# Kernel tuning notes

Measured on AMD Instinct MI355X. Metric: run time of the kernel, lower is better.

Reference implementation:

```python
import jax, jax.numpy as jnp
import numpy as np

# Config (lite version of KimiK2): 2 layers, dim 2048, 16 heads x 128, MLA latent rank 512,
# 4 experts / top-2, SwiGLU inter dim 1024, vocab 32000, batch 2, seq 1024.
DEPTH, DIM, H, HD, R, DFF, E, TOPK, V, B, S = 2, 2048, 16, 128, 512, 1024, 4, 2, 32000, 2, 1024
EPS = 1e-6


def rmsnorm(x, w):
    var = jnp.mean(jnp.square(x), axis=-1, keepdims=True)
    return x * jax.lax.rsqrt(var + EPS) * w


def setup_inputs() -> dict:
    key = jax.random.key(0)
    ks = jax.random.split(key, 16)
    sd = 0.02
    d = {
        'x_tokens': jax.random.randint(ks[0], (B, S), 0, V),
        'emb': jax.random.normal(ks[1], (V, DIM), jnp.float32) * sd,
        'embed_norm_w': jnp.ones((DIM,), jnp.float32),
        # per-layer stacked params (leading axis DEPTH)
        'norm_w': jnp.ones((DEPTH, DIM), jnp.float32),
        'Wq': jax.random.normal(ks[2], (DEPTH, DIM, H * HD), jnp.float32) * sd,
        'Wdkv': jax.random.normal(ks[3], (DEPTH, DIM, R), jnp.float32) * sd,
        'Wuk': jax.random.normal(ks[4], (DEPTH, R, H * HD), jnp.float32) * sd,
        'Wuv': jax.random.normal(ks[5], (DEPTH, R, H * HD), jnp.float32) * sd,
        'Wo': jax.random.normal(ks[6], (DEPTH, H * HD, DIM), jnp.float32) * sd,
        'Wg': jax.random.normal(ks[7], (DEPTH, DIM, E), jnp.float32) * sd,
        'W1': jax.random.normal(ks[8], (DEPTH, E, DIM, DFF), jnp.float32) * sd,
        'W3': jax.random.normal(ks[9], (DEPTH, E, DIM, DFF), jnp.float32) * sd,
        'W2': jax.random.normal(ks[10], (DEPTH, E, DFF, DIM), jnp.float32) * sd,
        'head_norm_w': jnp.ones((DIM,), jnp.float32),
        'head_W': jax.random.normal(ks[11], (DIM, V), jnp.float32) * sd,
        'head_b': jnp.zeros((V,), jnp.float32),
    }
    return d


def mla(x, Wq, Wdkv, Wuk, Wuv, Wo):
    # Multi-head latent attention: queries from x, K/V from a low-rank latent c.
    Bq, Sq, _ = x.shape
    q = (x @ Wq).reshape(Bq, Sq, H, HD)
    c = x @ Wdkv                                   # [B,S,R] compressed KV latent
    k = (c @ Wuk).reshape(Bq, Sq, H, HD)
    v = (c @ Wuv).reshape(Bq, Sq, H, HD)
    scores = jnp.einsum('bqhd,bkhd->bhqk', q, k) / jnp.sqrt(jnp.float32(HD))
    a = jax.nn.softmax(scores, axis=-1)            # block never passes a mask -> full attention
    o = jnp.einsum('bhqk,bkhd->bqhd', a, v).reshape(Bq, Sq, H * HD)
    return o @ Wo


def moe(x, Wg, W1, W3, W2):
    # x: [B,S,D] -> flatten tokens. Dense-over-experts (E=4) with top-k masked gates.
    Bq, Sq, Dq = x.shape
    xt = x.reshape(Bq * Sq, Dq)                    # [T,D]
    gate = jax.nn.softmax(xt @ Wg, axis=-1)        # [T,E]
    topv, topi = jax.lax.top_k(gate, TOPK)
    topv = topv / jnp.sum(topv, axis=-1, keepdims=True)
    gw = jnp.zeros_like(gate).at[jnp.arange(xt.shape[0])[:, None], topi].set(topv)  # [T,E]
    h = jnp.einsum('td,edf->etf', xt, W1)
    g = jnp.einsum('td,edf->etf', xt, W3)
    eo = jnp.einsum('etf,efd->etd', jax.nn.silu(h) * g, W2)
    out = jnp.einsum('etd,te->td', eo, gw)
    return out.reshape(Bq, Sq, Dq)


def reference(x_tokens, emb, embed_norm_w, norm_w, Wq, Wdkv, Wuk, Wuv, Wo, Wg, W1, W3, W2, head_norm_w, head_W, head_b):
    h = emb[x_tokens]
    h = rmsnorm(h, embed_norm_w)

    def layer(h, p):
        nw, wq, wdkv, wuk, wuv, wo, wg, w1, w3, w2 = p
        h = h + mla(rmsnorm(h, nw), wq, wdkv, wuk, wuv, wo)
        # NOTE: same norm weight reused pre-MoE, as in the torch module
        h = h + moe(rmsnorm(h, nw), wg, w1, w3, w2)
        return h, None

    h, _ = jax.lax.scan(layer, h, (norm_w, Wq, Wdkv, Wuk, Wuv, Wo, Wg, W1, W3, W2))
    return rmsnorm(h, head_norm_w) @ head_W + head_b
```

## Files before the change

kernel.cpp:

```cpp
#include <hip/hip_runtime.h>
#include <hip/hip_bf16.h>

typedef __hip_bfloat16 bf16;
typedef __bf16 bf16x8 __attribute__((ext_vector_type(8)));
typedef float f32x4 __attribute__((ext_vector_type(4)));
typedef unsigned short u16;
typedef unsigned int u32;
typedef __attribute__((address_space(1))) const void* gptr_t;
typedef __attribute__((address_space(3))) void* lptr_t;

static constexpr int TOKS = 2048, DM = 2048, RL = 512, DF = 1024, SQ = 1024, NV = 32000;
static constexpr int CAP = 1536;
static constexpr long PL_X  = (long)TOKS * DM;
static constexpr long PL_C  = (long)TOKS * RL;
static constexpr long PL_VT = 2l * 16 * 128 * 1024;
static constexpr long M4 = 4l * 1024 * 1024;
static constexpr long M2 = 2l * 1024 * 1024;

__device__ __forceinline__ float b2f(bf16 x){ return __bfloat162float(x); }
__device__ __forceinline__ bf16  f2b(float x){ return __float2bfloat16(x); }
__device__ __forceinline__ void split1(float x, u16& h, u16& l){
  bf16 hb = f2b(x);
  float r = x - b2f(hb);
  bf16 lb = f2b(r);
  h = *(u16*)&hb; l = *(u16*)&lb;
}

__device__ __forceinline__ float block_red(float v, int op){
  __shared__ float red[4];
  const int lane = threadIdx.x & 63, wv = threadIdx.x >> 6;
  #pragma unroll
  for (int off = 32; off > 0; off >>= 1){
    float o = __shfl_down(v, off, 64);
    v = op ? fmaxf(v, o) : v + o;
  }
  __syncthreads();
  if (lane == 0) red[wv] = v;
  __syncthreads();
  float r = red[0];
  #pragma unroll
  for (int i = 1; i < 4; ++i) r = op ? fmaxf(r, red[i]) : r + red[i];
  return r;
}

__global__ __launch_bounds__(256)
void embed_norm_k(const int* __restrict__ toks, const float* __restrict__ emb,
                  const float* __restrict__ w, float* __restrict__ h){
  const int t = blockIdx.x;
  const long tok = toks[t];
  const int base = threadIdx.x * 8;
  const float* ep = emb + tok * (long)DM + base;
  float4 va = *(const float4*)ep, vb = *(const float4*)(ep + 4);
  float v[8] = {va.x, va.y, va.z, va.w, vb.x, vb.y, vb.z, vb.w};
  float ss = 0.f;
  #pragma unroll
  for (int i = 0; i < 8; ++i) ss += v[i]*v[i];
  ss = block_red(ss, 0);
  const float inv = rsqrtf(ss / DM + 1e-6f);
  float4 wa = *(const float4*)(w + base), wb4 = *(const float4*)(w + base + 4);
  float wv[8] = {wa.x, wa.y, wa.z, wa.w, wb4.x, wb4.y, wb4.z, wb4.w};
  float* hp = h + (long)t * DM + base;
  #pragma unroll
  for (int i = 0; i < 8; ++i) hp[i] = v[i] * inv * wv[i];
}

__global__ __launch_bounds__(256)
void rmsnorm_planes_k(const float* __restrict__ h, const float* __restrict__ w,
                      u16* __restrict__ hi, u16* __restrict__ lo){
  const int t = blockIdx.x;
  const int base = threadIdx.x * 8;
  const float* hp = h + (long)t * DM + base;
  float4 va = *(const float4*)hp, vb = *(const float4*)(hp + 4);
  float v[8] = {va.x, va.y, va.z, va.w, vb.x, vb.y, vb.z, vb.w};
  float ss = 0.f;
  #pragma unroll
  for (int i = 0; i < 8; ++i) ss += v[i]*v[i];
  ss = block_red(ss, 0);
  const float inv = rsqrtf(ss / DM + 1e-6f);
  float4 wa = *(const float4*)(w + base), wb4 = *(const float4*)(w + base + 4);
  float wv[8] = {wa.x, wa.y, wa.z, wa.w, wb4.x, wb4.y, wb4.z, wb4.w};
  u16 hvv[8], lvv[8];
  #pragma unroll
  for (int i = 0; i < 8; ++i) split1(v[i] * inv * wv[i], hvv[i], lvv[i]);
  *(int4*)(hi + (long)t * DM + base) = *(const int4*)hvv;
  *(int4*)(lo + (long)t * DM + base) = *(const int4*)lvv;
}

__global__ __launch_bounds__(256)
void gate_k(const float* __restrict__ h, const float* __restrict__ nw,
            const float* __restrict__ Wg, float* __restrict__ gw){
  const int t = blockIdx.x;
  const int base = threadIdx.x * 8;
  const float* hp = h + (long)t * DM + base;
  float4 va = *(const float4*)hp, vb = *(const float4*)(hp + 4);
  float v[8] = {va.x, va.y, va.z, va.w, vb.x, vb.y, vb.z, vb.w};
  float ss = 0.f;
  #pragma unroll
  for (int i = 0; i < 8; ++i) ss += v[i]*v[i];
  ss = block_red(ss, 0);
  const float inv = rsqrtf(ss / DM + 1e-6f);
  float a[4] = {0.f, 0.f, 0.f, 0.f};
  #pragma unroll
  for (int i = 0; i < 8; ++i){
    const float xv = v[i] * inv * nw[base + i];
    #pragma unroll
    for (int e = 0; e < 4; ++e) a[e] += xv * Wg[(base + i)*4 + e];
  }
  #pragma unroll
  for (int e = 0; e < 4; ++e) a[e] = block_red(a[e], 0);
  if (threadIdx.x == 0){
    int i1 = 0;
    for (int e = 1; e < 4; ++e) if (a[e] > a[i1]) i1 = e;
    int i2 = -1;
    for (int e = 0; e < 4; ++e){ if (e == i1) continue; if (i2 < 0 || a[e] > a[i2]) i2 = e; }
    float g[4];
    const float m = fmaxf(fmaxf(a[0], a[1]), fmaxf(a[2], a[3]));
    float s = 0.f;
    for (int e = 0; e < 4; ++e){ g[e] = __expf(a[e] - m); s += g[e]; }
    for (int e = 0; e < 4; ++e) g[e] /= s;
    const float ns = g[i1] + g[i2];
    float* op = gw + (long)t * 4;
    op[0] = 0.f; op[1] = 0.f; op[2] = 0.f; op[3] = 0.f;
    op[i1] = g[i1] / ns; op[i2] = g[i2] / ns;
  }
}

__global__ __launch_bounds__(256)
void build_lists_k(const float* __restrict__ gw, int* __restrict__ idx, int* __restrict__ cnt){
  const int e = threadIdx.x >> 6, lane = threadIdx.x & 63;
  int base = 0;
  for (int t0 = 0; t0 < TOKS; t0 += 64){
    const int t = t0 + lane;
    const bool sel = gw[(long)t * 4 + e] > 0.f;
    const unsigned long long m = __ballot(sel);
    const int pos = __popcll(m & ((1ull << lane) - 1ull));
    if (sel && base + pos < CAP) idx[e * CAP + base + pos] = t;
    base += (int)__popcll(m);
  }
  if (lane == 0) cnt[e] = base < CAP ? base : CAP;
}

__global__ __launch_bounds__(256)
void gather2_k(const u16* __restrict__ xph, const int* __restrict__ idx,
               const int* __restrict__ cnt, int ebase, u16* __restrict__ xg){
  const int e = blockIdx.x / CAP, r = blockIdx.x % CAP;
  if (r >= cnt[ebase + e]) return;
  const long t = idx[(long)(ebase + e) * CAP + r];
  const int c = threadIdx.x * 8;
  const long dst = ((long)e * 2 * CAP + r) * DM + c;
  *(int4*)(xg + dst) = *(const int4*)(xph + t * DM + c);
  *(int4*)(xg + dst + (long)CAP * DM) = *(const int4*)(xph + PL_X + t * DM + c);
}

__global__ __launch_bounds__(256)
void gatherb_k(const u16* __restrict__ xph, const int* __restrict__ idx,
               const int* __restrict__ cnt, u16* __restrict__ xgb){
  const int e = blockIdx.x / CAP, r = blockIdx.x % CAP;
  if (r >= cnt[e]) return;
  const long t = idx[(long)e * CAP + r];
  const int c = threadIdx.x * 8;
  *(int4*)(xgb + ((long)e * CAP + r) * DM + c) = *(const int4*)(xph + t * DM + c);
}

__global__ __launch_bounds__(256)
void softmax_pack_k(float* __restrict__ pf){
  const long row = blockIdx.x;
  const float* pr = pf + row * SQ;
  const int base = threadIdx.x * 4;
  float4 v4 = *(const float4*)(pr + base);
  float v[4] = {v4.x, v4.y, v4.z, v4.w};
  float m = fmaxf(fmaxf(v[0], v[1]), fmaxf(v[2], v[3]));
  m = block_red(m, 1);
  float s = 0.f;
  #pragma unroll
  for (int i = 0; i < 4; ++i){ v[i] = __expf(v[i] - m); s += v[i]; }
  s = block_red(s, 0);
  const float inv = 1.f / s;
  u16 hv[4], lv[4];
  #pragma unroll
  for (int i = 0; i < 4; ++i) split1(v[i] * inv, hv[i], lv[i]);
  u16* out = (u16*)pf + row * 2048;
  *(int2*)(out + base) = *(const int2*)hv;
  *(int2*)(out + 1024 + base) = *(const int2*)lv;
}

__global__ __launch_bounds__(256)
void swiglu_pack_k(float* __restrict__ h1, const float* __restrict__ h3){
  const int t = threadIdx.x;
  const long r = (long)blockIdx.x * 2 + (t >> 7);
  const int col = (t & 127) * 8;
  const float* p1 = h1 + r * 1024 + col;
  const float* p3 = h3 + r * 1024 + col;
  float4 a0 = *(const float4*)p1, a1 = *(const float4*)(p1 + 4);
  float4 b0 = *(const float4*)p3, b1 = *(const float4*)(p3 + 4);
  float a[8] = {a0.x, a0.y, a0.z, a0.w, a1.x, a1.y, a1.z, a1.w};
  float b[8] = {b0.x, b0.y, b0.z, b0.w, b1.x, b1.y, b1.z, b1.w};
  u16 hv[8], lv[8];
  #pragma unroll
  for (int j = 0; j < 8; ++j){
    const float y = (a[j] / (1.f + __expf(-a[j]))) * b[j];
    split1(y, hv[j], lv[j]);
  }
  __syncthreads();
  u16* out = (u16*)h1 + r * 2048;
  *(int4*)(out + col) = *(const int4*)hv;
  *(int4*)(out + 1024 + col) = *(const int4*)lv;
}

__global__ __launch_bounds__(256)
void swiglu_bk(bf16* __restrict__ h1, const bf16* __restrict__ h3){
  const long i = ((long)blockIdx.x * 256 + threadIdx.x) * 8;
  union { int4 i4; bf16 b[8]; } x, y;
  x.i4 = *(const int4*)(h1 + i);
  y.i4 = *(const int4*)(h3 + i);
  #pragma unroll
  for (int j = 0; j < 8; ++j){
    const float a = b2f(x.b[j]);
    const float b = b2f(y.b[j]);
    x.b[j] = f2b((a / (1.f + __expf(-a))) * b);
  }
  *(int4*)(h1 + i) = x.i4;
}

__global__ __launch_bounds__(256)
void tsplit_k(const float* __restrict__ in, long inz, int ldin,
              u16* __restrict__ oh, u16* __restrict__ ol, long outz, int ldout, int ntx){
  __shared__ u16 lh[64][72], ll[64][72];
  const int z = blockIdx.z;
  in += (long)z * inz; oh += (long)z * outz; ol += (long)z * outz;
  const int bx = blockIdx.x % ntx, by = blockIdx.x / ntx;
  const int k0 = by * 64, n0 = bx * 64;
  const int t = threadIdx.x;
  {
    const int r = t >> 2, cb = (t & 3) * 16;
    const float* ip = in + (long)(k0 + r) * ldin + n0 + cb;
    #pragma unroll
    for (int i = 0; i < 16; i += 4){
      float4 v = *(const float4*)(ip + i);
      float a[4] = {v.x, v.y, v.z, v.w};
      #pragma unroll
      for (int j = 0; j < 4; ++j){
        u16 hv, lv; split1(a[j], hv, lv);
        lh[r][cb + i + j] = hv; ll[r][cb + i + j] = lv;
      }
    }
  }
  __syncthreads();
  {
    const int n = t >> 2, kb = (t & 3) * 16;
    u16 hv[16], lv[16];
    #pragma unroll
    for (int i = 0; i < 16; ++i){ hv[i] = lh[kb + i][n]; lv[i] = ll[kb + i][n]; }
    u16* po = oh + (long)(n0 + n) * ldout + k0 + kb;
    u16* pl = ol + (long)(n0 + n) * ldout + k0 + kb;
    *(int4*)po = *(const int4*)hv; *(int4*)(po + 8) = *(const int4*)(hv + 8);
    *(int4*)pl = *(const int4*)lv; *(int4*)(pl + 8) = *(const int4*)(lv + 8);
  }
}

__global__ __launch_bounds__(256)
void tconv_k(const float* __restrict__ in, long inz, int ldin,
             bf16* __restrict__ out, long outz, int ldout, int ntx){
  __shared__ u16 lh[64][72];
  const int z = blockIdx.z;
  in += (long)z * inz; out += (long)z * outz;
  const int bx = blockIdx.x % ntx, by = blockIdx.x / ntx;
  const int k0 = by * 64, n0 = bx * 64;
  const int t = threadIdx.x;
  {
    const int r = t >> 2, cb = (t & 3) * 16;
    const float* ip = in + (long)(k0 + r) * ldin + n0 + cb;
    #pragma unroll
    for (int i = 0; i < 16; i += 4){
      float4 v = *(const float4*)(ip + i);
      float a[4] = {v.x, v.y, v.z, v.w};
      #pragma unroll
      for (int j = 0; j < 4; ++j){ bf16 hb = f2b(a[j]); lh[r][cb + i + j] = *(u16*)&hb; }
    }
  }
  __syncthreads();
  {
    const int n = t >> 2, kb = (t & 3) * 16;
    u16 hv[16];
    #pragma unroll
    for (int i = 0; i < 16; ++i) hv[i] = lh[kb + i][n];
    u16* po = (u16*)out + (long)(n0 + n) * ldout + k0 + kb;
    *(int4*)po = *(const int4*)hv; *(int4*)(po + 8) = *(const int4*)(hv + 8);
  }
}

__device__ __forceinline__ int swz64(int r, int c){
  return ((((c >> 3) + r) & 7) << 3) | (c & 7);
}
__device__ __forceinline__ int swz2(int r, int c){
  return ((((c >> 3) + (r >> 1)) & 3) << 3) | (c & 7);
}
__device__ __forceinline__ int2 tile_xy(int ny){
  const int nwg = gridDim.x;
  const int wid = blockIdx.x;
  const int q = nwg >> 3, r = nwg & 7;
  const int xcd = wid & 7, pos = wid >> 3;
  const int lid = (xcd < r) ? (xcd*(q+1) + pos) : (r*(q+1) + (xcd - r)*q + pos);
  return make_int2(lid / ny, lid % ny);
}

__device__ __forceinline__ void stage64(const u16* src, int ld, int rbase, int k0,
                                        u16* lp, int sub, int lane){
  const int r = sub * 8 + (lane >> 3);
  const int cs = ((lane & 7) - r) & 7;
  const u16* g = src + (long)(rbase + r) * ld + k0 + cs * 8;
  __builtin_amdgcn_global_load_lds((gptr_t)g, (lptr_t)(lp + sub * 512), 16, 0, 0);
}
__device__ __forceinline__ void stage32(const u16* src, int ld, int rbase, int k0,
                                        u16* lp, int sub, int lane){
  const int r = sub * 16 + (lane >> 2);
  const int cs = ((lane & 3) - (r >> 1)) & 3;
  const u16* g = src + (long)(rbase + r) * ld + k0 + cs * 8;
  __builtin_amdgcn_global_load_lds((gptr_t)g, (lptr_t)(lp + sub * 512), 16, 0, 0);
}

template<int MT, int OM>
__global__ __launch_bounds__(256)
void gemms_nt(const u16* __restrict__ Ah, const u16* __restrict__ Al, long ab, int lda,
              const u16* __restrict__ Bh, const u16* __restrict__ Bl, long bb, int ldb,
              void* __restrict__ Cv, long cb, int ldc, long cpl,
              int K, float scale, const float* __restrict__ aux, int gst, int ny,
              const int* __restrict__ rowmap, const int* __restrict__ cntp)
{
  __shared__ __align__(16) u16 ash[MT*32][64], asl[MT*32][64];
  __shared__ __align__(16) u16 bsh[128][64], bsl[128][64];
  const int z = blockIdx.z;
  Ah += (long)z * ab; Al += (long)z * ab;
  Bh += (long)z * bb; Bl += (long)z * bb;
  const int2 tt = tile_xy(ny);
  const int m0 = tt.y * (MT*32), n0 = tt.x * 128;
  int cntv = 1 << 30;
  if (cntp){ cntv = cntp[z]; if (m0 >= cntv) return; }
  const int tid = threadIdx.x, lane = tid & 63, wv = tid >> 6;
  const int wr = (wv >> 1) * (MT*16), wc = (wv & 1) * 64;
  const int fr = lane & 15, fk = (lane >> 4) * 8;

  f32x4 acc[MT][4] = {};
  constexpr int AI4 = MT * 4;

  for (int k0 = 0; k0 < K; k0 += 64){
    __syncthreads();
    #pragma unroll
    for (int ii = 0; ii < 2*AI4 + 32; ++ii){
      if ((ii & 3) != wv) continue;
      if (ii < AI4)             stage64(Ah, lda, m0, k0, &ash[0][0], ii, lane);
      else if (ii < 2*AI4)      stage64(Al, lda, m0, k0, &asl[0][0], ii - AI4, lane);
      else if (ii < 2*AI4 + 16) stage64(Bh, ldb, n0, k0, &bsh[0][0], ii - 2*AI4, lane);
      else                      stage64(Bl, ldb, n0, k0, &bsl[0][0], ii - 2*AI4 - 16, lane);
    }
    __syncthreads();
    bf16x8 ahf[MT][2], alf[MT][2], bhf[4][2], blf[4][2];
    #pragma unroll
    for (int mi = 0; mi < MT; ++mi){
      const int rr = wr + mi * 16 + fr;
      #pragma unroll
      for (int ks = 0; ks < 2; ++ks){
        const int sc = swz64(rr, ks * 32 + fk);
        ahf[mi][ks] = *(const bf16x8*)&ash[rr][sc];
        alf[mi][ks] = *(const bf16x8*)&asl[rr][sc];
      }
    }
    #pragma unroll
    for (int ni = 0; ni < 4; ++ni){
      const int rr = wc + ni * 16 + fr;
      #pragma unroll
      for (int ks = 0; ks < 2; ++ks){
        const int sc = swz64(rr, ks * 32 + fk);
        bhf[ni][ks] = *(const bf16x8*)&bsh[rr][sc];
        blf[ni][ks] = *(const bf16x8*)&bsl[rr][sc];
      }
    }
    #pragma unroll
    for (int mi = 0; mi < MT; ++mi)
      #pragma unroll
      for (int ni = 0; ni < 4; ++ni)
        #pragma unroll
        for (int ks = 0; ks < 2; ++ks){
          acc[mi][ni] = __builtin_amdgcn_mfma_f32_16x16x32_bf16(ahf[mi][ks], bhf[ni][ks], acc[mi][ni], 0, 0, 0);
          acc[mi][ni] = __builtin_amdgcn_mfma_f32_16x16x32_bf16(ahf[mi][ks], blf[ni][ks], acc[mi][ni], 0, 0, 0);
          acc[mi][ni] = __builtin_amdgcn_mfma_f32_16x16x32_bf16(alf[mi][ks], bhf[ni][ks], acc[mi][ni], 0, 0, 0);
        }
  }

  const int crow = (lane >> 4) * 4, ccol = lane & 15;
  #pragma unroll
  for (int mi = 0; mi < MT; ++mi){
    #pragma unroll
    for (int ni = 0; ni < 4; ++ni){
      const int gm0 = m0 + wr + mi * 16 + crow;
      const int gn = n0 + wc + ni * 16 + ccol;
      if (OM == 5){
        u16 hv[4], lv[4];
        #pragma unroll
        for (int j = 0; j < 4; ++j) split1(acc[mi][ni][j], hv[j], lv[j]);
        const long off = (((long)(gm0 >> 10) * 16 + (gn >> 7)) * 128 + (gn & 127)) * 1024 + (gm0 & 1023);
        u16* vt = (u16*)Cv;
        *(int2*)(vt + off) = *(const int2*)hv;
        *(int2*)(vt + cpl + off) = *(const int2*)lv;
      } else if (OM == 6){
        #pragma unroll
        for (int j = 0; j < 4; ++j){
          const int row = gm0 + j;
          if (row < cntv){
            const long t = rowmap[(long)z * CAP + row];
            ((float*)Cv)[t * ldc + gn] += aux[t * gst] * acc[mi][ni][j];
          }
        }
      } else {
        #pragma unroll
        for (int j = 0; j < 4; ++j){
          const long off = (long)z * cb + (long)(gm0 + j) * ldc + gn;
          const float v = acc[mi][ni][j];
          if (OM == 0)      ((float*)Cv)[off] = v * scale;
          else if (OM == 1) ((float*)Cv)[off] += v;
          else if (OM == 3) ((float*)Cv)[off] += aux[(long)(gm0 + j) * gst] * v;
          else { u16 hv, lv; split1(v, hv, lv); ((u16*)Cv)[off] = hv; ((u16*)Cv)[off + cpl] = lv; }
        }
      }
    }
  }
}

template<int MT, int OM>
__global__ __launch_bounds__(256)
void gemmb_nt(const bf16* __restrict__ A, long ab, int lda,
              const bf16* __restrict__ B, long bb, int ldb,
              void* __restrict__ Cv, long cb, int ldc,
              int K, const float* __restrict__ aux, int gst, int ny,
              const int* __restrict__ rowmap, const int* __restrict__ cntp)
{
  __shared__ __align__(16) u16 a_lds[MT*32][32];
  __shared__ __align__(16) u16 b_lds[128][32];
  const int z = blockIdx.z;
  A += (long)z * ab; B += (long)z * bb;
  const int2 tt = tile_xy(ny);
  const int m0 = tt.y * (MT*32), n0 = tt.x * 128;
  int cntv = 1 << 30;
  if (cntp){ cntv = cntp[z]; if (m0 >= cntv) return; }
  const int tid = threadIdx.x, lane = tid & 63, wv = tid >> 6;
  const int wr = (wv >> 1) * (MT*16), wc = (wv & 1) * 64;
  const int fr = lane & 15, fk = (lane >> 4) * 8;

  f32x4 acc[MT][4] = {};
  constexpr int AI = MT * 2;

  for (int k0 = 0; k0 < K; k0 += 32){
    __syncthreads();
    #pragma unroll
    for (int ii = 0; ii < AI + 8; ++ii){
      if ((ii & 3) != wv) continue;
      if (ii < AI) stage32((const u16*)A, lda, m0, k0, &a_lds[0][0], ii, lane);
      else         stage32((const u16*)B, ldb, n0, k0, &b_lds[0][0], ii - AI, lane);
    }
    __syncthreads();
    bf16x8 af[MT], bfv[4];
    #pragma unroll
    for (int mi = 0; mi < MT; ++mi){
      const int rr = wr + mi * 16 + fr;
      af[mi] = *(const bf16x8*)&a_lds[rr][swz2(rr, fk)];
    }
    #pragma unroll
    for (int ni = 0; ni < 4; ++ni){
      const int rr = wc + ni * 16 + fr;
      bfv[ni] = *(const bf16x8*)&b_lds[rr][swz2(rr, fk)];
    }
    #pragma unroll
    for (int mi = 0; mi < MT; ++mi)
      #pragma unroll
      for (int ni = 0; ni < 4; ++ni)
        acc[mi][ni] = __builtin_amdgcn_mfma_f32_16x16x32_bf16(af[mi], bfv[ni], acc[mi][ni], 0, 0, 0);
  }

  const int crow = (lane >> 4) * 4, ccol = lane & 15;
  #pragma unroll
  for (int mi = 0; mi < MT; ++mi){
    #pragma unroll
    for (int ni = 0; ni < 4; ++ni){
      const int gm0 = m0 + wr + mi * 16 + crow;
      const int gn = n0 + wc + ni * 16 + ccol;
      #pragma unroll
      for (int j = 0; j < 4; ++j){
        const float v = acc[mi][ni][j];
        if (OM == 7){
          const int row = gm0 + j;
          if (row < cntv){
            const long t = rowmap[(long)z * CAP + row];
            atomicAdd(&((float*)Cv)[t * ldc + gn], aux[t * gst + z] * v);
          }
        } else {
          const long off = (long)z * cb + (long)(gm0 + j) * ldc + gn;
          if (OM == 0)      ((bf16*)Cv)[off] = f2b(v);
          else if (OM == 2) ((float*)Cv)[off] = v + aux[gn];
          else              atomicAdd(&((float*)Cv)[off], aux[(long)(gm0 + j) * gst + z] * v);
        }
      }
    }
  }
}

extern "C" void kernel_launch(void* const* d_in, const int* in_sizes, int n_in,
                              void* d_out, int out_size, void* d_ws, size_t ws_size,
                              hipStream_t stream)
{
  (void)in_sizes; (void)n_in; (void)out_size; (void)ws_size;
  const int*   toks = (const int*)d_in[0];
  const float* emb  = (const float*)d_in[1];
  const float* enw  = (const float*)d_in[2];
  const float* nw   = (const float*)d_in[3];
  const float* Wq   = (const float*)d_in[4];
  const float* Wdkv = (const float*)d_in[5];
  const float* Wuk  = (const float*)d_in[6];
  const float* Wuv  = (const float*)d_in[7];
  const float* Wo   = (const float*)d_in[8];
  const float* Wg   = (const float*)d_in[9];
  const float* W1   = (const float*)d_in[10];
  const float* W3   = (const float*)d_in[11];
  const float* W2   = (const float*)d_in[12];
  const float* hnw  = (const float*)d_in[13];
  const float* hW   = (const float*)d_in[14];
  const float* hb   = (const float*)d_in[15];

  const size_t MB = 1ull << 20;
  char* ws = (char*)d_ws;
  float* h    = (float*)(ws);
  float* gw   = (float*)(ws + 16*MB);
  int*   idx  = (int*)(ws + 16*MB + 128*1024);
  int*   cnt  = (int*)(ws + 16*MB + 256*1024);
  u16*   xph  = (u16*)(ws + 17*MB);
  u16*   wpl  = (u16*)(ws + 33*MB);
  u16*   qph  = (u16*)(ws + 49*MB);
  u16*   cph  = (u16*)(ws + 65*MB);
  u16*   kph  = (u16*)(ws + 69*MB);
  u16*   vtp  = (u16*)(ws + 85*MB);
  u16*   oph  = (u16*)(ws + 101*MB);
  float* pf   = (float*)(ws + 17*MB);
  u16*   xg   = (u16*)(ws + 49*MB);
  float* h1f  = (float*)(ws + 73*MB);
  float* h3f  = (float*)(ws + 85*MB);
  bf16*  wT   = (bf16*)(ws + 33*MB);
  u16*   xgb  = (u16*)(ws + 49*MB);
  bf16*  h1b  = (bf16*)(ws + 73*MB);
  bf16*  h3b  = (bf16*)(ws + 85*MB);
  bf16*  whT  = (bf16*)(ws + 33*MB);

  const float qscale = 0.08838834764831845f;

  embed_norm_k<<<TOKS, 256, 0, stream>>>(toks, emb, enw, h);

  for (int l = 0; l < 2; ++l){
    const float* nwl = nw + (long)l * DM;
    rmsnorm_planes_k<<<TOKS, 256, 0, stream>>>(h, nwl, xph, xph + PL_X);

    tsplit_k<<<1024, 256, 0, stream>>>(Wq + (long)l*DM*DM, 0, DM, wpl, wpl + M4, 0, DM, 32);
    gemms_nt<2,4><<<dim3(512,1,1), 256, 0, stream>>>(xph, xph + PL_X, 0, DM, wpl, wpl + M4, 0, DM,
        qph, 0, DM, PL_X, DM, 1.f, nullptr, 0, 32, nullptr, nullptr);
    tsplit_k<<<256, 256, 0, stream>>>(Wdkv + (long)l*DM*RL, 0, RL, wpl, wpl + M2, 0, DM, 8);
    gemms_nt<2,4><<<dim3(128,1,1), 256, 0, stream>>>(xph, xph + PL_X, 0, DM, wpl, wpl + M2, 0, DM,
        cph, 0, RL, PL_C, DM, 1.f, nullptr, 0, 32, nullptr, nullptr);
    tsplit_k<<<256, 256, 0, stream>>>(Wuk + (long)l*RL*DM, 0, DM, wpl, wpl + M2, 0, RL, 32);
    gemms_nt<2,4><<<dim3(512,1,1), 256, 0, stream>>>(cph, cph + PL_C, 0, RL, wpl, wpl + M2, 0, RL,
        kph, 0, DM, PL_X, RL, 1.f, nullptr, 0, 32, nullptr, nullptr);
    tsplit_k<<<256, 256, 0, stream>>>(Wuv + (long)l*RL*DM, 0, DM, wpl, wpl + M2, 0, RL, 32);
    gemms_nt<2,5><<<dim3(512,1,1), 256, 0, stream>>>(cph, cph + PL_C, 0, RL, wpl, wpl + M2, 0, RL,
        vtp, 0, 0, PL_VT, RL, 1.f, nullptr, 0, 32, nullptr, nullptr);

    for (int b = 0; b < 2; ++b){
      for (int hg = 0; hg < 2; ++hg){
        const long qo = (long)b*SQ*DM + hg*1024;
        gemms_nt<4,0><<<dim3(64,1,8), 256, 0, stream>>>(qph + qo, qph + PL_X + qo, 128, DM,
            kph + qo, kph + PL_X + qo, 128, DM,
            pf, (long)SQ*SQ, SQ, 0, 128, qscale, nullptr, 0, 8, nullptr, nullptr);
        softmax_pack_k<<<8*SQ, 256, 0, stream>>>(pf);
        const long vo = ((long)b*16 + hg*8) * 128 * 1024;
        gemms_nt<1,4><<<dim3(32,1,8), 256, 0, stream>>>((const u16*)pf, (const u16*)pf + 1024,
            1024l*2048, 2048,
            vtp + vo, vtp + PL_VT + vo, 128l*1024, 1024,
            oph + (long)b*SQ*DM + hg*1024, 128, DM, PL_X, SQ, 1.f, nullptr, 0, 32, nullptr, nullptr);
      }
    }

    tsplit_k<<<1024, 256, 0, stream>>>(Wo + (long)l*DM*DM, 0, DM, wpl, wpl + M4, 0, DM, 32);
    gemms_nt<2,1><<<dim3(512,1,1), 256, 0, stream>>>(oph, oph + PL_X, 0, DM, wpl, wpl + M4, 0, DM,
        h, 0, DM, 0, DM, 1.f, nullptr, 0, 32, nullptr, nullptr);

    gate_k<<<TOKS, 256, 0, stream>>>(h, nwl, Wg + (long)l*DM*4, gw);
    build_lists_k<<<1, 256, 0, stream>>>(gw, idx, cnt);
    rmsnorm_planes_k<<<TOKS, 256, 0, stream>>>(h, nwl, xph, xph + PL_X);

    if (l == 0){
      for (int p2 = 0; p2 < 2; ++p2){
        const int ebase = p2 * 2;
        const long wo13 = ((long)l*4 + ebase) * (long)DM * DF;
        gather2_k<<<2*CAP, 256, 0, stream>>>(xph, idx, cnt, ebase, xg);
        tsplit_k<<<dim3(512,1,2), 256, 0, stream>>>(W1 + wo13, (long)DM*DF, DF, wpl, wpl + M4, M2, DM, 16);
        gemms_nt<2,0><<<dim3(192,1,2), 256, 0, stream>>>(xg, xg + (long)CAP*DM, 2l*CAP*DM, DM,
            wpl, wpl + M4, M2, DM, h1f, (long)CAP*DF, DF, 0, DM, 1.f, nullptr, 0, 24,
            nullptr, cnt + ebase);
        tsplit_k<<<dim3(512,1,2), 256, 0, stream>>>(W3 + wo13, (long)DM*DF, DF, wpl, wpl + M4, M2, DM, 16);
        gemms_nt<2,0><<<dim3(192,1,2), 256, 0, stream>>>(xg, xg + (long)CAP*DM, 2l*CAP*DM, DM,
            wpl, wpl + M4, M2, DM, h3f, (long)CAP*DF, DF, 0, DM, 1.f, nullptr, 0, 24,
            nullptr, cnt + ebase);
        swiglu_pack_k<<<CAP, 256, 0, stream>>>(h1f, h3f);
        tsplit_k<<<dim3(512,1,2), 256, 0, stream>>>(W2 + ((long)l*4 + ebase)*(long)DF*DM, (long)DF*DM, DM,
            wpl, wpl + M4, M2, DF, 32);
        for (int ei = 0; ei < 2; ++ei){
          gemms_nt<2,6><<<dim3(384,1,1), 256, 0, stream>>>(
              (const u16*)h1f + (long)ei*CAP*2048, (const u16*)h1f + (long)ei*CAP*2048 + 1024,
              0, 2048, wpl + (long)ei*M2, wpl + M4 + (long)ei*M2, 0, DF,
              h, 0, DM, 0, DF, 1.f, gw + ebase + ei, 4, 24,
              idx + (ebase + ei)*CAP, cnt + ebase + ei);
        }
      }
    } else {
      gatherb_k<<<4*CAP, 256, 0, stream>>>(xph, idx, cnt, xgb);
      tconv_k<<<dim3(512,1,4), 256, 0, stream>>>(W1 + (long)l*4*DM*DF, (long)DM*DF, DF, wT, M2, DM, 16);
      gemmb_nt<2,0><<<dim3(192,1,4), 256, 0, stream>>>((const bf16*)xgb, (long)CAP*DM, DM, wT, M2, DM,
          h1b, (long)CAP*DF, DF, DM, nullptr, 0, 24, nullptr, cnt);
      tconv_k<<<dim3(512,1,4), 256, 0, stream>>>(W3 + (long)l*4*DM*DF, (long)DM*DF, DF, wT, M2, DM, 16);
      gemmb_nt<2,0><<<dim3(192,1,4), 256, 0, stream>>>((const bf16*)xgb, (long)CAP*DM, DM, wT, M2, DM,
          h3b, (long)CAP*DF, DF, DM, nullptr, 0, 24, nullptr, cnt);
      swiglu_bk<<<(4*CAP*DF)/2048, 256, 0, stream>>>(h1b, h3b);
      tconv_k<<<dim3(512,1,4), 256, 0, stream>>>(W2 + (long)l*4*DF*DM, (long)DF*DM, DM, wT, M2, DF, 32);
      gemmb_nt<2,7><<<dim3(384,1,4), 256, 0, stream>>>(h1b, (long)CAP*DF, DF, wT, M2, DF,
          h, 0, DM, DF, gw, 4, 24, idx, cnt);
    }
  }

  rmsnorm_planes_k<<<TOKS, 256, 0, stream>>>(h, hnw, xph, xph + PL_X);
  for (int half = 0; half < 2; ++half){
    tconv_k<<<8000, 256, 0, stream>>>(hW + half*16000, 0, NV, whT, 0, DM, 250);
    gemmb_nt<4,2><<<dim3(2000,1,1), 256, 0, stream>>>((const bf16*)xph, 0, DM, whT, 0, DM,
        (float*)d_out + half*16000, 0, NV, DM, hb + half*16000, 0, 16, nullptr, nullptr);
  }
}
```

Before: 2.176 ms.

## Triple-buffer LDS staging in bf16 GEMM with async prefetch two tiles ahead

The bf16 NT GEMM kernel now keeps three LDS buffers for the A and B tiles and issues global-to-LDS loads two K-steps ahead. It waits on vmcnt counters instead of a full sync, so MFMA work on the current tile overlaps with memory loads of later tiles. The cost is three times the LDS footprint, which may lower occupancy, and hand-written waitcnt and barrier code that assumes each wave issues a fixed number of loads.

```diff
diff --git a/kernel.cpp b/kernel.cpp
--- a/kernel.cpp
+++ b/kernel.cpp
@@ -317,6 +317,20 @@
   const int cs = ((lane & 3) - (r >> 1)) & 3;
   const u16* g = src + (long)(rbase + r) * ld + k0 + cs * 8;
   __builtin_amdgcn_global_load_lds((gptr_t)g, (lptr_t)(lp + sub * 512), 16, 0, 0);
+}
+
+template<int N> __device__ __forceinline__ void wait_vmcnt(){
+  if constexpr (N == 0) asm volatile("s_waitcnt vmcnt(0)" ::: "memory");
+  else if constexpr (N == 3) asm volatile("s_waitcnt vmcnt(3)" ::: "memory");
+  else if constexpr (N == 4) asm volatile("s_waitcnt vmcnt(4)" ::: "memory");
+  __builtin_amdgcn_sched_barrier(0);
+}
+__device__ __forceinline__ void barrier_raw(){
+  __builtin_amdgcn_sched_barrier(0);
+  asm volatile("" ::: "memory");
+  __builtin_amdgcn_s_barrier();
+  asm volatile("" ::: "memory");
+  __builtin_amdgcn_sched_barrier(0);
 }
 
 template<int MT, int OM>
@@ -434,8 +448,8 @@
               int K, const float* __restrict__ aux, int gst, int ny,
               const int* __restrict__ rowmap, const int* __restrict__ cntp)
 {
-  __shared__ __align__(16) u16 a_lds[MT*32][32];
-  __shared__ __align__(16) u16 b_lds[128][32];
+  __shared__ __align__(16) u16 a_lds[3][MT*32][32];
+  __shared__ __align__(16) u16 b_lds[3][128][32];
   const int z = blockIdx.z;
   A += (long)z * ab; B += (long)z * bb;
   const int2 tt = tile_xy(ny);
@@ -448,32 +462,50 @@
 
   f32x4 acc[MT][4] = {};
   constexpr int AI = MT * 2;
-
+  constexpr int TOT = AI + 8;
+  constexpr int IPW = TOT / 4;
+
+  auto STAGE = [&](int bf, int k0){
+    #pragma unroll
+    for (int ii = 0; ii < TOT; ++ii){
+      if ((ii & 3) != wv) continue;
+      if (ii < AI) stage32((const u16*)A, lda, m0, k0, &a_lds[bf][0][0], ii, lane);
+      else         stage32((const u16*)B, ldb, n0, k0, &b_lds[bf][0][0], ii - AI, lane);
+    }
+  };
+
+  STAGE(0, 0);
+  STAGE(1, 32);
+  int cur = 0;
   for (int k0 = 0; k0 < K; k0 += 32){
-    __syncthreads();
-    #pragma unroll
-    for (int ii = 0; ii < AI + 8; ++ii){
-      if ((ii & 3) != wv) continue;
-      if (ii < AI) stage32((const u16*)A, lda, m0, k0, &a_lds[0][0], ii, lane);
-      else         stage32((const u16*)B, ldb, n0, k0, &b_lds[0][0], ii - AI, lane);
-    }
-    __syncthreads();
+    if (k0 + 64 < K){
+      int nb = cur + 2; if (nb >= 3) nb -= 3;
+      STAGE(nb, k0 + 64);
+      wait_vmcnt<IPW>();
+    } else if (k0 + 32 < K){
+      wait_vmcnt<IPW>();
+    } else {
+      wait_vmcnt<0>();
+    }
+    barrier_raw();
     bf16x8 af[MT], bfv[4];
     #pragma unroll
     for (int mi = 0; mi < MT; ++mi){
       const int rr = wr + mi * 16 + fr;
-      af[mi] = *(const bf16x8*)&a_lds[rr][swz2(rr, fk)];
+      af[mi] = *(const bf16x8*)&a_lds[cur][rr][swz2(rr, fk)];
     }
     #pragma unroll
     for (int ni = 0; ni < 4; ++ni){
       const int rr = wc + ni * 16 + fr;
-      bfv[ni] = *(const bf16x8*)&b_lds[rr][swz2(rr, fk)];
+      bfv[ni] = *(const bf16x8*)&b_lds[cur][rr][swz2(rr, fk)];
     }
     #pragma unroll
     for (int mi = 0; mi < MT; ++mi)
       #pragma unroll
       for (int ni = 0; ni < 4; ++ni)
         acc[mi][ni] = __builtin_amdgcn_mfma_f32_16x16x32_bf16(af[mi], bfv[ni], acc[mi][ni], 0, 0, 0);
+    barrier_raw();
+    cur += 1; if (cur >= 3) cur -= 3;
   }
 
   const int crow = (lane >> 4) * 4, ccol = lane & 15;
```

New measurement: 2.235 ms. 1.03x slower.
